# Kernel optimization log

Hardware: AMD Instinct MI355X
Metric: run time of the kernel (lower is better)

Reference implementation:

```python
import jax, jax.numpy as jnp
import numpy as np


def setup_inputs() -> dict:
    key = jax.random.key(0)
    k1, k2, k3, k4 = jax.random.split(key, 4)
    B, S, H, D = 4, 2048, 1024, 1024
    X = jax.random.normal(k1, (B, S, H), dtype=jnp.float32)
    # nn.Linear weight stored as [out, in]; we store as [in, out] for x @ W
    scale = 1.0 / np.sqrt(H)
    Wq = jax.random.normal(k2, (H, D), dtype=jnp.float32) * scale
    Wk = jax.random.normal(k3, (H, D), dtype=jnp.float32) * scale
    Wv = jax.random.normal(k4, (H, D), dtype=jnp.float32) * scale
    return {"X": X, "Wq": Wq, "Wk": Wk, "Wv": Wv}


def reference(X, Wq, Wk, Wv):
    B, S, H = X.shape
    q = X @ Wq  # [B, S, D]
    k = X @ Wk
    v = X @ Wv
    D = k.shape[-1]
    scores = jnp.einsum('bqd,bkd->bqk', q, k) / jnp.sqrt(jnp.float32(D))
    causal = jnp.tril(jnp.ones((S, S), dtype=bool))  # block_size mask sliced to S
    scores = jnp.where(causal, scores, -jnp.inf)
    weights = jax.nn.softmax(scores, axis=-1)  # dropout p=0.0 -> identity
    return jnp.einsum('bqk,bkd->bqd', weights, v)
```

## Files before the change

### kernel.cpp

```cpp
#include <hip/hip_runtime.h>

#define AS1 __attribute__((address_space(1)))
#define AS3 __attribute__((address_space(3)))

typedef __attribute__((ext_vector_type(8))) short short8;
typedef __attribute__((ext_vector_type(4))) float floatx4;

__device__ __forceinline__ short f2bf(float f) {
  union { float f; unsigned u; } v; v.f = f;
  return (short)((v.u + 0x7fffu + ((v.u >> 16) & 1u)) >> 16);
}
__device__ __forceinline__ float bf2f(short s) {
  union { unsigned u; float f; } v; v.u = ((unsigned)(unsigned short)s) << 16;
  return v.f;
}

__device__ __forceinline__ void gload_lds16(const void* g, void* l) {
  __builtin_amdgcn_global_load_lds((const AS1 unsigned*)g, (AS3 unsigned*)l, 16, 0, 0);
}

__device__ __forceinline__ void stage128x64(const short* __restrict__ G, long rowBase, long ld,
                                            int kBase, short* lds, int lane, int wave) {
  const short* gb = G + rowBase * ld + (long)kBase + (long)(lane >> 3) * ld + (lane & 7) * 8;
#pragma unroll
  for (int j = 0; j < 4; ++j) {
    int c = wave * 4 + j;
    gload_lds16(gb + (long)c * 8 * ld, lds + c * 512);
  }
}

__device__ __forceinline__ void mfma_step(const short* lA, const short* lB, floatx4 acc[4][4],
                                          int lane, int wm, int wn) {
#pragma unroll
  for (int kk = 0; kk < 64; kk += 32) {
    short8 a[4], b[4];
    int kq = kk + (lane >> 4) * 8;
#pragma unroll
    for (int i = 0; i < 4; ++i) {
      a[i] = *(const short8*)(lA + (wm * 64 + i * 16 + (lane & 15)) * 64 + kq);
      b[i] = *(const short8*)(lB + (wn * 64 + i * 16 + (lane & 15)) * 64 + kq);
    }
#pragma unroll
    for (int i = 0; i < 4; ++i)
#pragma unroll
      for (int j = 0; j < 4; ++j)
        acc[i][j] = __builtin_amdgcn_mfma_f32_16x16x32_bf16(a[i], b[j], acc[i][j], 0, 0, 0);
  }
}

__device__ const unsigned char PAIR_LUT[136] = {
  0x40,0x41,0x42,0x43,0x50,0x51,0x52,0x53,0x60,0x61,0x62,0x63,0x70,0x71,0x72,0x73,
  0x80,0x81,0x82,0x83,0x90,0x91,0x92,0x93,0xA0,0xA1,0xA2,0xA3,0xB0,0xB1,0xB2,0xB3,
  0x84,0x85,0x86,0x87,0x94,0x95,0x96,0x97,0xA4,0xA5,0xA6,0xA7,0xB4,0xB5,0xB6,0xB7,
  0xC0,0xC1,0xC2,0xC3,0xD0,0xD1,0xD2,0xD3,0xE0,0xE1,0xE2,0xE3,0xF0,0xF1,0xF2,0xF3,
  0xC4,0xC5,0xC6,0xC7,0xD4,0xD5,0xD6,0xD7,0xE4,0xE5,0xE6,0xE7,0xF4,0xF5,0xF6,0xF7,
  0xC8,0xC9,0xCA,0xCB,0xD8,0xD9,0xDA,0xDB,0xE8,0xE9,0xEA,0xEB,0xF8,0xF9,0xFA,0xFB,
  0x00,0x10,0x11,0x20,0x21,0x22,0x30,0x31,0x32,0x33,
  0x44,0x54,0x55,0x64,0x65,0x66,0x74,0x75,0x76,0x77,
  0x88,0x98,0x99,0xA8,0xA9,0xAA,0xB8,0xB9,0xBA,0xBB,
  0xCC,0xDC,0xDD,0xEC,0xED,0xEE,0xFC,0xFD,0xFE,0xFF
};

__global__ void prep_inputs(const float* __restrict__ X, const float* __restrict__ Wq,
                            const float* __restrict__ Wk, const float* __restrict__ Wv,
                            short* __restrict__ Xb, short* __restrict__ Wt,
                            float* __restrict__ l) {
  __shared__ float t[32][33];
  if (blockIdx.x < 8192) {
    long i = ((long)blockIdx.x * 256 + threadIdx.x) * 4;
    float4 v = *(const float4*)(X + i);
    short4 o;
    o.x = f2bf(v.x); o.y = f2bf(v.y); o.z = f2bf(v.z); o.w = f2bf(v.w);
    *(short4*)(Xb + i) = o;
  } else if (blockIdx.x < 11264) {
    int idx = blockIdx.x - 8192;
    int z = idx >> 10, rem = idx & 1023;
    int bx = rem >> 5, by = rem & 31;
    const float* W = z == 0 ? Wq : (z == 1 ? Wk : Wv);
    short* O = Wt + (long)z * 1024 * 1024;
    int tx = threadIdx.x & 31, ty = threadIdx.x >> 5;
    int x = bx * 32 + tx;
    int y0 = by * 32;
    for (int j = ty; j < 32; j += 8)
      t[j][tx] = W[(long)(y0 + j) * 1024 + x];
    __syncthreads();
    int x2 = by * 32 + tx;
    int y2 = bx * 32;
    for (int j = ty; j < 32; j += 8)
      O[(long)(y2 + j) * 1024 + x2] = f2bf(t[tx][j]);
  } else {
    l[(blockIdx.x - 11264) * 256 + threadIdx.x] = 0.0f;
  }
}

#define LOFF(b, m, h) ((((b) * 2 + (m)) * 2 + (h)) * 8192)
#define MEMFENCE() asm volatile("" ::: "memory")
#define SBAR() do { MEMFENCE(); __builtin_amdgcn_s_barrier(); MEMFENCE(); } while (0)
#define SCHEDB() __builtin_amdgcn_sched_barrier(0)

__device__ __forceinline__ void stage_half(const short* __restrict__ g, short* l, int wv) {
  gload_lds16(g, l + wv * 512);
  gload_lds16(g + 65536, l + 4096 + wv * 512);
}

__device__ __forceinline__ short8 lds_rd(const short* l, int row, int kk, int lane) {
  const int r = row + (lane & 15);
  const int c = (kk + ((lane >> 4) << 3)) ^ ((lane & 7) << 3);
  return *(const short8*)(l + r * 64 + c);
}

__global__ __launch_bounds__(512, 2) void gemm_qkv(const short* __restrict__ Xb,
                                                   const short* __restrict__ Wt,
                                                   short* __restrict__ Q, short* __restrict__ K2,
                                                   short* __restrict__ Vt) {
  __shared__ __align__(16) short lds[65536];
  const int tid = threadIdx.x;
  const int lane = tid & 63, wv = tid >> 6;
  const int wm = wv >> 2, wn = wv & 3;

  const int bid = blockIdx.x;
  const int xcd = bid & 7, w = bid >> 3;
  const int mt = xcd * 4 + (w / 12);
  const int ng = w % 12;
  const int z = ng >> 2;
  const long mBase = (long)mt * 256;
  const long nBase = (long)(ng & 3) * 256;
  const short* Bm = Wt + (long)z * 1048576;

  const int r0 = tid >> 3;
  const int cc = ((tid & 7) ^ (r0 & 7)) << 3;
  const short* gA = Xb + (mBase + r0) * 1024 + cc;
  const short* gB = Bm + (nBase + r0) * 1024 + cc;

  floatx4 acc[8][4];
  const floatx4 zero = {0.f, 0.f, 0.f, 0.f};
#pragma unroll
  for (int i = 0; i < 8; ++i)
#pragma unroll
    for (int j = 0; j < 4; ++j) acc[i][j] = zero;

  stage_half(gA, lds + LOFF(0, 0, 0), wv);
  stage_half(gA + 131072, lds + LOFF(0, 0, 1), wv);
  stage_half(gB, lds + LOFF(0, 1, 0), wv);
  stage_half(gB + 131072, lds + LOFF(0, 1, 1), wv);
  stage_half(gA + 64, lds + LOFF(1, 0, 0), wv);
  stage_half(gA + 64 + 131072, lds + LOFF(1, 0, 1), wv);
  stage_half(gB + 64, lds + LOFF(1, 1, 0), wv);
  asm volatile("s_waitcnt vmcnt(6)" ::: "memory");
  SBAR();

#pragma unroll 2
  for (int t = 0; t < 16; ++t) {
    const int buf = t & 1;
    const short* Ab = lds + LOFF(buf, 0, wm);
    const short* Bb = lds + LOFF(buf, 1, (wn >> 1));
    const int brow = (wn & 1) * 64;
    short8 a0[4][2], a1[4][2], bq[2][2];

    bq[0][0] = lds_rd(Bb, brow + 0 * 16, 0, lane);
    bq[1][0] = lds_rd(Bb, brow + 1 * 16, 0, lane);
#pragma unroll
    for (int f = 0; f < 4; ++f) a0[f][0] = lds_rd(Ab, f * 16, 0, lane);
    bq[0][1] = lds_rd(Bb, brow + 0 * 16, 32, lane);
    bq[1][1] = lds_rd(Bb, brow + 1 * 16, 32, lane);
#pragma unroll
    for (int f = 0; f < 4; ++f) a0[f][1] = lds_rd(Ab, f * 16, 32, lane);
    if (t < 15) stage_half(gB + (t + 1) * 64 + 131072, lds + LOFF(buf ^ 1, 1, 1), wv);
    SBAR();
    asm volatile("s_waitcnt lgkmcnt(6)" ::: "memory");
    SCHEDB();
    __builtin_amdgcn_s_setprio(1);
#pragma unroll
    for (int f = 0; f < 4; ++f)
#pragma unroll
      for (int n = 0; n < 2; ++n)
        acc[f][n] = __builtin_amdgcn_mfma_f32_16x16x32_bf16(a0[f][0], bq[n][0], acc[f][n], 0, 0, 0);
    asm volatile("s_waitcnt lgkmcnt(0)" ::: "memory");
    SCHEDB();
#pragma unroll
    for (int f = 0; f < 4; ++f)
#pragma unroll
      for (int n = 0; n < 2; ++n)
        acc[f][n] = __builtin_amdgcn_mfma_f32_16x16x32_bf16(a0[f][1], bq[n][1], acc[f][n], 0, 0, 0);
    __builtin_amdgcn_s_setprio(0);
    SBAR();

#pragma unroll
    for (int f = 0; f < 4; ++f) a1[f][0] = lds_rd(Ab, 64 + f * 16, 0, lane);
#pragma unroll
    for (int f = 0; f < 4; ++f) a1[f][1] = lds_rd(Ab, 64 + f * 16, 32, lane);
    SBAR();
    asm volatile("s_waitcnt lgkmcnt(4)" ::: "memory");
    SCHEDB();
    __builtin_amdgcn_s_setprio(1);
#pragma unroll
    for (int f = 0; f < 4; ++f)
#pragma unroll
      for (int n = 0; n < 2; ++n)
        acc[4 + f][n] = __builtin_amdgcn_mfma_f32_16x16x32_bf16(a1[f][0], bq[n][0], acc[4 + f][n], 0, 0, 0);
    asm volatile("s_waitcnt lgkmcnt(0)" ::: "memory");
    SCHEDB();
#pragma unroll
    for (int f = 0; f < 4; ++f)
#pragma unroll
      for (int n = 0; n < 2; ++n)
        acc[4 + f][n] = __builtin_amdgcn_mfma_f32_16x16x32_bf16(a1[f][1], bq[n][1], acc[4 + f][n], 0, 0, 0);
    __builtin_amdgcn_s_setprio(0);
    SBAR();

    bq[0][0] = lds_rd(Bb, brow + 2 * 16, 0, lane);
    bq[1][0] = lds_rd(Bb, brow + 3 * 16, 0, lane);
    bq[0][1] = lds_rd(Bb, brow + 2 * 16, 32, lane);
    bq[1][1] = lds_rd(Bb, brow + 3 * 16, 32, lane);
    if (t < 14) stage_half(gA + (t + 2) * 64, lds + LOFF(buf, 0, 0), wv);
    SBAR();
    asm volatile("s_waitcnt lgkmcnt(2)" ::: "memory");
    SCHEDB();
    __builtin_amdgcn_s_setprio(1);
#pragma unroll
    for (int f = 0; f < 4; ++f)
#pragma unroll
      for (int n = 0; n < 2; ++n)
        acc[f][2 + n] = __builtin_amdgcn_mfma_f32_16x16x32_bf16(a0[f][0], bq[n][0], acc[f][2 + n], 0, 0, 0);
    asm volatile("s_waitcnt lgkmcnt(0)" ::: "memory");
    SCHEDB();
#pragma unroll
    for (int f = 0; f < 4; ++f)
#pragma unroll
      for (int n = 0; n < 2; ++n)
        acc[f][2 + n] = __builtin_amdgcn_mfma_f32_16x16x32_bf16(a0[f][1], bq[n][1], acc[f][2 + n], 0, 0, 0);
    __builtin_amdgcn_s_setprio(0);
    SBAR();

    if (t < 14) {
      stage_half(gA + (t + 2) * 64 + 131072, lds + LOFF(buf, 0, 1), wv);
      stage_half(gB + (t + 2) * 64, lds + LOFF(buf, 1, 0), wv);
    }
    SBAR();
    __builtin_amdgcn_s_setprio(1);
#pragma unroll
    for (int f = 0; f < 4; ++f)
#pragma unroll
      for (int n = 0; n < 2; ++n)
        acc[4 + f][2 + n] = __builtin_amdgcn_mfma_f32_16x16x32_bf16(a1[f][0], bq[n][0], acc[4 + f][2 + n], 0, 0, 0);
#pragma unroll
    for (int f = 0; f < 4; ++f)
#pragma unroll
      for (int n = 0; n < 2; ++n)
        acc[4 + f][2 + n] = __builtin_amdgcn_mfma_f32_16x16x32_bf16(a1[f][1], bq[n][1], acc[4 + f][2 + n], 0, 0, 0);
    __builtin_amdgcn_s_setprio(0);
    if (t < 14) { asm volatile("s_waitcnt vmcnt(6)" ::: "memory"); }
    else        { asm volatile("s_waitcnt vmcnt(0)" ::: "memory"); }
    SBAR();
  }

  if (z < 2) {
    short* outp = (z == 0) ? Q : K2;
#pragma unroll
    for (int f = 0; f < 8; ++f)
#pragma unroll
      for (int n = 0; n < 4; ++n) {
        const int col = (int)nBase + wn * 64 + n * 16 + (lane & 15);
#pragma unroll
        for (int rr = 0; rr < 4; ++rr) {
          const long m = mBase + wm * 128 + f * 16 + ((lane >> 4) << 2) + rr;
          outp[m * 1024 + col] = f2bf(acc[f][n][rr]);
        }
      }
  } else {
    const long bz = mBase >> 11;
    const int sB = (int)(mBase & 2047);
#pragma unroll
    for (int f = 0; f < 8; ++f) {
      const int s0 = sB + wm * 128 + f * 16 + ((lane >> 4) << 2);
#pragma unroll
      for (int n = 0; n < 4; ++n) {
        const int col = (int)nBase + wn * 64 + n * 16 + (lane & 15);
        short4 o;
        o.x = f2bf(acc[f][n][0]); o.y = f2bf(acc[f][n][1]);
        o.z = f2bf(acc[f][n][2]); o.w = f2bf(acc[f][n][3]);
        *(short4*)(Vt + ((bz * 1024 + col) * 2048 + s0)) = o;
      }
    }
  }
}

__global__ __launch_bounds__(256, 4) void scores_exp(const short* __restrict__ Q,
                                                     const short* __restrict__ Kk,
                                                     short* __restrict__ E, float* __restrict__ l) {
  __shared__ short lbuf[16384];
  short* lA = lbuf;
  short* lB = lbuf + 8192;
  const int lane = threadIdx.x & 63, wave = threadIdx.x >> 6;
  const int wm = wave >> 1, wn = wave & 1;
  const int b = blockIdx.y;

  const int r = blockIdx.x & 7, w = blockIdx.x >> 3;
  const int code = PAIR_LUT[r * 17 + w];
  const int qt = code >> 4, kt = code & 15;

  const long rowQ = (long)b * 2048 + (long)qt * 128;
  const long rowK = (long)b * 2048 + (long)kt * 128;

  floatx4 acc[4][4];
  const floatx4 zero = {0.f, 0.f, 0.f, 0.f};
#pragma unroll
  for (int i = 0; i < 4; ++i)
#pragma unroll
    for (int j = 0; j < 4; ++j) acc[i][j] = zero;

  for (int it = 0; it < 16; ++it) {
    stage128x64(Q, rowQ, 1024, it * 64, lA, lane, wave);
    stage128x64(Kk, rowK, 1024, it * 64, lB, lane, wave);
    __syncthreads();
    mfma_step(lA, lB, acc, lane, wm, wn);
    __syncthreads();
  }

  float* lrow = l + (long)b * 2048;
#pragma unroll
  for (int i = 0; i < 4; ++i) {
#pragma unroll
    for (int rr = 0; rr < 4; ++rr) {
      int ri = wm * 64 + i * 16 + (lane >> 4) * 4 + rr;
      int qrow = qt * 128 + ri;
      float psum = 0.f;
#pragma unroll
      for (int j = 0; j < 4; ++j) {
        int ci = wn * 64 + j * 16 + (lane & 15);
        int col = kt * 128 + ci;
        float sc = acc[i][j][rr] * 0.03125f;
        float e = (col <= qrow) ? __expf(sc) : 0.0f;
        short eb = f2bf(e);
        lbuf[ri * 128 + ((((ci >> 3) ^ (ri & 15)) << 3) | (ci & 7))] = eb;
        psum += bf2f(eb);
      }
      for (int m = 1; m < 16; m <<= 1) psum += __shfl_xor(psum, m, 64);
      if ((lane & 15) == 0) atomicAdd(&lrow[qrow], psum);
    }
  }
  __syncthreads();

  short* Eb = E + (long)b * 4194304;
  const long ebase = (long)(qt * 128) * 2048 + kt * 128;
#pragma unroll
  for (int pp = 0; pp < 8; ++pp) {
    int g = pp * 256 + threadIdx.x;
    int row = g >> 4, c = g & 15;
    short8 v = *(const short8*)(lbuf + row * 128 + ((c ^ (row & 15)) << 3));
    *(short8*)(Eb + ebase + (long)row * 2048 + c * 8) = v;
  }
}

__global__ __launch_bounds__(256, 4) void pv_gemm(const short* __restrict__ E,
                                                  const short* __restrict__ Vt,
                                                  const float* __restrict__ l,
                                                  float* __restrict__ part,
                                                  float* __restrict__ out) {
  __shared__ short lA[128 * 64], lB[128 * 64];
  const int lane = threadIdx.x & 63, wave = threadIdx.x >> 6;
  const int wm = wave >> 1, wn = wave & 1;
  const int xx = blockIdx.x;
  const int dt = xx / 24;
  const int within = xx % 24;
  const int r = within & 7, wsel = within >> 3;
  const int b = blockIdx.y;

  int qt, it0, it1, mode;
  if (wsel == 2) {
    qt = r; it0 = 0; it1 = (qt + 1) * 2; mode = 0;
  } else {
    qt = 15 - r;
    const int T = (qt + 1) * 2, c0 = T >> 1;
    if (wsel == 0) { it0 = 0;  it1 = c0; mode = 1; }
    else           { it0 = c0; it1 = T;  mode = 2; }
  }

  const short* Eb = E + (long)b * 2048 * 2048;
  const short* Vb = Vt + (long)b * 1024 * 2048;
  const float* lrow = l + (long)b * 2048;

  floatx4 acc[4][4];
  const floatx4 zero = {0.f, 0.f, 0.f, 0.f};
#pragma unroll
  for (int i = 0; i < 4; ++i)
#pragma unroll
    for (int j = 0; j < 4; ++j) acc[i][j] = zero;

  for (int it = it0; it < it1; ++it) {
    stage128x64(Eb, (long)qt * 128, 2048, it * 64, lA, lane, wave);
    stage128x64(Vb, (long)dt * 128, 2048, it * 64, lB, lane, wave);
    __syncthreads();
    mfma_step(lA, lB, acc, lane, wm, wn);
    __syncthreads();
  }

  if (mode == 2) {
    float* P = part + ((((long)b * 8 + (qt - 8)) * 8 + dt) << 14);
#pragma unroll
    for (int i = 0; i < 4; ++i)
#pragma unroll
      for (int rr = 0; rr < 4; ++rr) {
        int ri = wm * 64 + i * 16 + (lane >> 4) * 4 + rr;
#pragma unroll
        for (int j = 0; j < 4; ++j) {
          int ci = wn * 64 + j * 16 + (lane & 15);
          P[ri * 128 + ci] = acc[i][j][rr];
        }
      }
  } else {
#pragma unroll
    for (int i = 0; i < 4; ++i)
#pragma unroll
      for (int rr = 0; rr < 4; ++rr) {
        int qrow = qt * 128 + wm * 64 + i * 16 + (lane >> 4) * 4 + rr;
        float scale = (mode == 0) ? 1.0f / lrow[qrow] : 1.0f;
#pragma unroll
        for (int j = 0; j < 4; ++j) {
          int d = dt * 128 + wn * 64 + j * 16 + (lane & 15);
          out[((long)b * 2048 + qrow) * 1024 + d] = acc[i][j][rr] * scale;
        }
      }
  }
}

__global__ void pv_reduce(float* __restrict__ out, const float* __restrict__ part,
                          const float* __restrict__ l) {
  const int idx = blockIdx.x;
  const int b = idx >> 10;
  const int row = 1024 + (idx & 1023);
  const int t = threadIdx.x;
  const int dt = t >> 5, dl = (t << 2) & 127;
  const float inv = 1.0f / l[((long)b << 11) + row];
  const long pbase = ((((long)b * 8 + ((row >> 7) - 8)) * 8 + dt) << 14) + ((row & 127) << 7) + dl;
  const long obase = (((long)b * 2048 + row) << 10) + (t << 2);
  float4 o = *(const float4*)(out + obase);
  float4 p = *(const float4*)(part + pbase);
  o.x = (o.x + p.x) * inv; o.y = (o.y + p.y) * inv;
  o.z = (o.z + p.z) * inv; o.w = (o.w + p.w) * inv;
  *(float4*)(out + obase) = o;
}

extern "C" void kernel_launch(void* const* d_in, const int* in_sizes, int n_in,
                              void* d_out, int out_size, void* d_ws, size_t ws_size,
                              hipStream_t stream) {
  const float* X  = (const float*)d_in[0];
  const float* Wq = (const float*)d_in[1];
  const float* Wk = (const float*)d_in[2];
  const float* Wv = (const float*)d_in[3];

  char* ws = (char*)d_ws;
  short* Xb = (short*)(ws);
  short* Wt = (short*)(ws + 16777216L);
  short* Q  = (short*)(ws + 23068672L);
  short* K2 = (short*)(ws + 39845888L);
  short* Vt = (short*)(ws + 56623104L);
  short* E  = (short*)(ws + 73400320L);
  float* l  = (float*)(ws + 106954752L);
  float* part = (float*)(ws);

  prep_inputs<<<11296, 256, 0, stream>>>(X, Wq, Wk, Wv, Xb, Wt, l);
  gemm_qkv<<<384, 512, 0, stream>>>(Xb, Wt, Q, K2, Vt);
  scores_exp<<<dim3(136, 4), 256, 0, stream>>>(Q, K2, E, l);
  pv_gemm<<<dim3(192, 4), 256, 0, stream>>>(E, Vt, l, part, (float*)d_out);
  pv_reduce<<<4096, 256, 0, stream>>>((float*)d_out, part, l);
}
```

Baseline: 238.8 us.

## Prefetch next-tile A fragments across iterations and drop redundant barriers in QKV GEMM

Restructures the QKV projection GEMM main loop so the A fragments for the next k-tile are read from LDS during the last MFMA phase of the current iteration, carried in registers across iterations. The per-iteration barrier count drops from several to two, and the vmcnt wait moves earlier. The goal is to hide LDS read latency behind MFMAs and cut synchronisation stalls. In exchange the new schedule depends on subtle buffer-reuse ordering, which risks races on LDS slots, and holding fragments live across iterations raises register pressure.

```diff
diff --git a/kernel.cpp b/kernel.cpp
--- a/kernel.cpp
+++ b/kernel.cpp
@@ -139,6 +139,8 @@
 #pragma unroll
     for (int j = 0; j < 4; ++j) acc[i][j] = zero;
 
+  short8 a0[4][2], a1[4][2], bq[2][2];
+
   stage_half(gA, lds + LOFF(0, 0, 0), wv);
   stage_half(gA + 131072, lds + LOFF(0, 0, 1), wv);
   stage_half(gB, lds + LOFF(0, 1, 0), wv);
@@ -148,26 +150,32 @@
   stage_half(gB + 64, lds + LOFF(1, 1, 0), wv);
   asm volatile("s_waitcnt vmcnt(6)" ::: "memory");
   SBAR();
+  {
+    const short* Ab0 = lds + LOFF(0, 0, wm);
+#pragma unroll
+    for (int f = 0; f < 4; ++f) a0[f][0] = lds_rd(Ab0, f * 16, 0, lane);
+#pragma unroll
+    for (int f = 0; f < 4; ++f) a0[f][1] = lds_rd(Ab0, f * 16, 32, lane);
+  }
 
 #pragma unroll 2
   for (int t = 0; t < 16; ++t) {
     const int buf = t & 1;
-    const short* Ab = lds + LOFF(buf, 0, wm);
-    const short* Bb = lds + LOFF(buf, 1, (wn >> 1));
+    const short* Ab  = lds + LOFF(buf, 0, wm);
+    const short* Bb  = lds + LOFF(buf, 1, (wn >> 1));
+    const short* AbN = lds + LOFF(buf ^ 1, 0, wm);
     const int brow = (wn & 1) * 64;
-    short8 a0[4][2], a1[4][2], bq[2][2];
-
-    bq[0][0] = lds_rd(Bb, brow + 0 * 16, 0, lane);
-    bq[1][0] = lds_rd(Bb, brow + 1 * 16, 0, lane);
-#pragma unroll
-    for (int f = 0; f < 4; ++f) a0[f][0] = lds_rd(Ab, f * 16, 0, lane);
-    bq[0][1] = lds_rd(Bb, brow + 0 * 16, 32, lane);
-    bq[1][1] = lds_rd(Bb, brow + 1 * 16, 32, lane);
-#pragma unroll
-    for (int f = 0; f < 4; ++f) a0[f][1] = lds_rd(Ab, f * 16, 32, lane);
+
+    bq[0][0] = lds_rd(Bb, brow, 0, lane);
+    bq[1][0] = lds_rd(Bb, brow + 16, 0, lane);
+    bq[0][1] = lds_rd(Bb, brow, 32, lane);
+    bq[1][1] = lds_rd(Bb, brow + 16, 32, lane);
+#pragma unroll
+    for (int f = 0; f < 4; ++f) a1[f][0] = lds_rd(Ab, 64 + f * 16, 0, lane);
+#pragma unroll
+    for (int f = 0; f < 4; ++f) a1[f][1] = lds_rd(Ab, 64 + f * 16, 32, lane);
     if (t < 15) stage_half(gB + (t + 1) * 64 + 131072, lds + LOFF(buf ^ 1, 1, 1), wv);
-    SBAR();
-    asm volatile("s_waitcnt lgkmcnt(6)" ::: "memory");
+    asm volatile("s_waitcnt lgkmcnt(8)" ::: "memory");
     SCHEDB();
     __builtin_amdgcn_s_setprio(1);
 #pragma unroll
@@ -175,31 +183,21 @@
 #pragma unroll
       for (int n = 0; n < 2; ++n)
         acc[f][n] = __builtin_amdgcn_mfma_f32_16x16x32_bf16(a0[f][0], bq[n][0], acc[f][n], 0, 0, 0);
+#pragma unroll
+    for (int f = 0; f < 4; ++f)
+#pragma unroll
+      for (int n = 0; n < 2; ++n)
+        acc[f][n] = __builtin_amdgcn_mfma_f32_16x16x32_bf16(a0[f][1], bq[n][1], acc[f][n], 0, 0, 0);
+    __builtin_amdgcn_s_setprio(0);
+
     asm volatile("s_waitcnt lgkmcnt(0)" ::: "memory");
     SCHEDB();
-#pragma unroll
-    for (int f = 0; f < 4; ++f)
-#pragma unroll
-      for (int n = 0; n < 2; ++n)
-        acc[f][n] = __builtin_amdgcn_mfma_f32_16x16x32_bf16(a0[f][1], bq[n][1], acc[f][n], 0, 0, 0);
-    __builtin_amdgcn_s_setprio(0);
-    SBAR();
-
-#pragma unroll
-    for (int f = 0; f < 4; ++f) a1[f][0] = lds_rd(Ab, 64 + f * 16, 0, lane);
-#pragma unroll
-    for (int f = 0; f < 4; ++f) a1[f][1] = lds_rd(Ab, 64 + f * 16, 32, lane);
-    SBAR();
-    asm volatile("s_waitcnt lgkmcnt(4)" ::: "memory");
-    SCHEDB();
     __builtin_amdgcn_s_setprio(1);
 #pragma unroll
     for (int f = 0; f < 4; ++f)
 #pragma unroll
       for (int n = 0; n < 2; ++n)
         acc[4 + f][n] = __builtin_amdgcn_mfma_f32_16x16x32_bf16(a1[f][0], bq[n][0], acc[4 + f][n], 0, 0, 0);
-    asm volatile("s_waitcnt lgkmcnt(0)" ::: "memory");
-    SCHEDB();
 #pragma unroll
     for (int f = 0; f < 4; ++f)
 #pragma unroll
@@ -208,13 +206,12 @@
     __builtin_amdgcn_s_setprio(0);
     SBAR();
 
-    bq[0][0] = lds_rd(Bb, brow + 2 * 16, 0, lane);
-    bq[1][0] = lds_rd(Bb, brow + 3 * 16, 0, lane);
-    bq[0][1] = lds_rd(Bb, brow + 2 * 16, 32, lane);
-    bq[1][1] = lds_rd(Bb, brow + 3 * 16, 32, lane);
+    bq[0][0] = lds_rd(Bb, brow + 32, 0, lane);
+    bq[1][0] = lds_rd(Bb, brow + 48, 0, lane);
+    bq[0][1] = lds_rd(Bb, brow + 32, 32, lane);
+    bq[1][1] = lds_rd(Bb, brow + 48, 32, lane);
     if (t < 14) stage_half(gA + (t + 2) * 64, lds + LOFF(buf, 0, 0), wv);
-    SBAR();
-    asm volatile("s_waitcnt lgkmcnt(2)" ::: "memory");
+    asm volatile("s_waitcnt lgkmcnt(0)" ::: "memory");
     SCHEDB();
     __builtin_amdgcn_s_setprio(1);
 #pragma unroll
@@ -222,21 +219,27 @@
 #pragma unroll
       for (int n = 0; n < 2; ++n)
         acc[f][2 + n] = __builtin_amdgcn_mfma_f32_16x16x32_bf16(a0[f][0], bq[n][0], acc[f][2 + n], 0, 0, 0);
-    asm volatile("s_waitcnt lgkmcnt(0)" ::: "memory");
-    SCHEDB();
 #pragma unroll
     for (int f = 0; f < 4; ++f)
 #pragma unroll
       for (int n = 0; n < 2; ++n)
         acc[f][2 + n] = __builtin_amdgcn_mfma_f32_16x16x32_bf16(a0[f][1], bq[n][1], acc[f][2 + n], 0, 0, 0);
     __builtin_amdgcn_s_setprio(0);
+    if (t < 14) { asm volatile("s_waitcnt vmcnt(2)" ::: "memory"); }
+    else        { asm volatile("s_waitcnt vmcnt(0)" ::: "memory"); }
     SBAR();
 
+    if (t < 15) {
+#pragma unroll
+      for (int f = 0; f < 4; ++f) a0[f][0] = lds_rd(AbN, f * 16, 0, lane);
+#pragma unroll
+      for (int f = 0; f < 4; ++f) a0[f][1] = lds_rd(AbN, f * 16, 32, lane);
+    }
     if (t < 14) {
       stage_half(gA + (t + 2) * 64 + 131072, lds + LOFF(buf, 0, 1), wv);
       stage_half(gB + (t + 2) * 64, lds + LOFF(buf, 1, 0), wv);
     }
-    SBAR();
+    SCHEDB();
     __builtin_amdgcn_s_setprio(1);
 #pragma unroll
     for (int f = 0; f < 4; ++f)
@@ -249,9 +252,6 @@
       for (int n = 0; n < 2; ++n)
         acc[4 + f][2 + n] = __builtin_amdgcn_mfma_f32_16x16x32_bf16(a1[f][1], bq[n][1], acc[4 + f][2 + n], 0, 0, 0);
     __builtin_amdgcn_s_setprio(0);
-    if (t < 14) { asm volatile("s_waitcnt vmcnt(6)" ::: "memory"); }
-    else        { asm volatile("s_waitcnt vmcnt(0)" ::: "memory"); }
-    SBAR();
   }
 
   if (z < 2) {
```

Result: no change. 236.4 us (-1.0%).
